# Kernel optimization log

Hardware: AMD Instinct MI355X
Metric: run time of the kernel (lower is better)

## Reference

```python
import jax, jax.numpy as jnp
import numpy as np

N_NODES = 50000
N_EDGES = 200000
IN_DIM = 16
NODE_DIM = 64
EDGE_DIM = 16
HIDDEN = 256
NUM_LAYERS = 4  # 1 NNConv + 3 GINConv


def setup_inputs() -> dict:
    key = jax.random.key(0)
    ks = jax.random.split(key, 20)
    s = 0.05
    inp = {
        "x": jax.random.normal(ks[0], (N_NODES, IN_DIM), dtype=jnp.float32),
        "edge_index": jax.random.randint(ks[1], (2, N_EDGES), 0, N_NODES, dtype=jnp.int64),
        "edge_attr": jax.random.normal(ks[2], (N_EDGES, EDGE_DIM), dtype=jnp.float32),
        # edge-NN (per-edge weight generator): attr_dim -> 256 -> 1024 -> in*out, ELU after each
        "enn_w1": jax.random.normal(ks[3], (EDGE_DIM, 256), dtype=jnp.float32) * s,
        "enn_b1": jnp.zeros((256,), dtype=jnp.float32),
        "enn_w2": jax.random.normal(ks[4], (256, 1024), dtype=jnp.float32) * s,
        "enn_b2": jnp.zeros((1024,), dtype=jnp.float32),
        "enn_w3": jax.random.normal(ks[5], (1024, IN_DIM * NODE_DIM), dtype=jnp.float32) * s,
        "enn_b3": jnp.zeros((IN_DIM * NODE_DIM,), dtype=jnp.float32),
        # NNConv root weight + bias
        "root_w": jax.random.normal(ks[6], (IN_DIM, NODE_DIM), dtype=jnp.float32) * s,
        "root_b": jnp.zeros((NODE_DIM,), dtype=jnp.float32),
        # 3 GIN MLPs (stacked): node_dim -> hidden -> hidden -> node_dim
        "gin_w1": jax.random.normal(ks[7], (3, NODE_DIM, HIDDEN), dtype=jnp.float32) * s,
        "gin_b1": jnp.zeros((3, HIDDEN), dtype=jnp.float32),
        "gin_w2": jax.random.normal(ks[8], (3, HIDDEN, HIDDEN), dtype=jnp.float32) * s,
        "gin_b2": jnp.zeros((3, HIDDEN), dtype=jnp.float32),
        "gin_w3": jax.random.normal(ks[9], (3, HIDDEN, NODE_DIM), dtype=jnp.float32) * s,
        "gin_b3": jnp.zeros((3, NODE_DIM), dtype=jnp.float32),
    }
    return inp


def _elu(x):
    return jax.nn.elu(x)


def reference(x, edge_index, edge_attr,
              enn_w1, enn_b1, enn_w2, enn_b2, enn_w3, enn_b3,
              root_w, root_b,
              gin_w1, gin_b1, gin_w2, gin_b2, gin_w3, gin_b3):
    src = edge_index[0]  # x_j (message source)
    dst = edge_index[1]  # i (aggregation target)

    # ---- Layer 0: NNConv with per-edge MLP-generated weights ----
    h = _elu(edge_attr @ enn_w1 + enn_b1)
    h = _elu(h @ enn_w2 + enn_b2)
    w_e = _elu(h @ enn_w3 + enn_b3).reshape(-1, IN_DIM, NODE_DIM)  # [E, in, out]
    msg = jnp.einsum('ei,eio->eo', x[src], w_e)                    # [E, node_dim]
    agg = jax.ops.segment_sum(msg, dst, num_segments=N_NODES)     # scatter-add
    x_cur = x @ root_w + agg + root_b                              # [N, node_dim]
    node_emb = [x_cur]

    # ---- Layers 1..3: GINConv (eps=0) with 3-layer MLP ----
    for l in range(NUM_LAYERS - 1):
        x_in = _elu(x_cur)
        nbr = jax.ops.segment_sum(x_in[src], dst, num_segments=N_NODES)
        h = x_in + nbr  # (1 + eps) * x + sum_j x_j, eps = 0
        h = _elu(h @ gin_w1[l] + gin_b1[l])
        h = _elu(h @ gin_w2[l] + gin_b2[l])
        x_cur = h @ gin_w3[l] + gin_b3[l]
        node_emb.append(x_cur)

    return jnp.stack(node_emb, axis=2)  # [N, node_dim, num_layers]
```

## Files before the change

### kernel.cpp

```cpp
#include <hip/hip_runtime.h>
#include <hip/hip_bf16.h>


#define NN 50000
#define EE 200000

typedef unsigned short u16;
typedef __attribute__((ext_vector_type(8))) short frag8;
typedef __attribute__((ext_vector_type(4))) float f32x4;

__device__ __forceinline__ float bf2f(u16 u) {
    union { unsigned int i; float f; } v; v.i = ((unsigned int)u) << 16; return v.f;
}
__device__ __forceinline__ u16 f2bf(float f) {
    union { float f; unsigned int i; } v; v.f = f;
    return (u16)((v.i + 0x7fffu + ((v.i >> 16) & 1u)) >> 16);
}
__device__ __forceinline__ float eluf(float v) {
    return v > 0.f ? v : __expf(v) - 1.f;
}

__global__ void probe_f32(const u16* __restrict__ raw, int* __restrict__ cnt) {
    int t = threadIdx.x;
    int c = 0;
    for (int j = t; j < 1024; j += 256) {
        unsigned e = (raw[j] >> 7) & 0xFF;
        if (e >= 0xBF) c++;
    }
    if (c) atomicAdd(cnt, c);
}
__global__ void cvt_bf16(const void* __restrict__ src, u16* __restrict__ dst, long n,
                         const int* __restrict__ cnt) {
    long i = (long)blockIdx.x * 256 + threadIdx.x;
    if (i >= n) return;
    if (*cnt >= 8) dst[i] = f2bf(((const float*)src)[i]);
    else           dst[i] = ((const u16*)src)[i];
}

__global__ void detect_idx64(const unsigned long long* __restrict__ p, int* __restrict__ flag) {
    long t = (long)blockIdx.x * 256 + threadIdx.x;
    if (t < EE) {
        unsigned long long v = p[t];
        if (v >> 31) atomicOr(flag, 1);
    }
}
__global__ void convert_idx(const void* __restrict__ raw, const int* __restrict__ flag,
                            int* __restrict__ s_out, int* __restrict__ d_out) {
    long t = (long)blockIdx.x * 256 + threadIdx.x;
    if (t >= EE) return;
    if (*flag) {
        const int* q = (const int*)raw;
        s_out[t] = q[t];
        d_out[t] = q[EE + t];
    } else {
        const long long* q = (const long long*)raw;
        s_out[t] = (int)q[t];
        d_out[t] = (int)q[EE + t];
    }
}

__global__ void transpose_bf16(const u16* __restrict__ in, u16* __restrict__ out, int K, int N) {
    long idx = (long)blockIdx.x * 256 + threadIdx.x;
    if (idx < (long)K * N) {
        int k = (int)(idx / N);
        int n = (int)(idx % N);
        out[(long)n * K + k] = in[idx];
    }
}

__global__ void edge_mlp1(const u16* __restrict__ attr, const u16* __restrict__ w1,
                          const u16* __restrict__ b1, u16* __restrict__ h1, int ce) {
    __shared__ u16 sa[256];
    const int t = threadIdx.x;
    const int e0 = blockIdx.x * 16;
    const int cnt = min(16, ce - e0);
    sa[t] = (t < cnt * 16) ? attr[(long)e0 * 16 + t] : (u16)0;
    float w[16];
    #pragma unroll
    for (int i = 0; i < 16; ++i) w[i] = bf2f(w1[i * 256 + t]);
    const float bb = bf2f(b1[t]);
    __syncthreads();
    for (int e = 0; e < cnt; ++e) {
        float v = bb;
        #pragma unroll
        for (int i = 0; i < 16; ++i) v += bf2f(sa[e * 16 + i]) * w[i];
        h1[(long)(e0 + e) * 256 + t] = f2bf(eluf(v));
    }
}

__device__ __forceinline__ void stage_tile(const u16* g, long row_base, long max_row,
                                           int kstride, int k0, u16* s, int t) {
    int wave = t >> 6;
    #pragma unroll
    for (int j = 0; j < 2; ++j) {
        int c = t + 256 * j;
        long r = row_base + (c >> 2);
        if (r > max_row) r = max_row;
        const u16* gp = g + r * (long)kstride + k0 + (c & 3) * 8;
        __builtin_amdgcn_global_load_lds(
            (__attribute__((address_space(1))) void*)(void*)gp,
            (__attribute__((address_space(3))) void*)((char*)s + wave * 1024 + j * 4096),
            16, 0, 0);
    }
}

__global__ __launch_bounds__(256)
void gemm_bt_bias_elu(const u16* __restrict__ A, const u16* __restrict__ BT,
                      const u16* __restrict__ bias, u16* __restrict__ C,
                      int M, int K, int N, int mpx, int lognt) {
    const int bid = blockIdx.x;
    const int xcd = bid & 7;
    const int j = bid >> 3;
    const int m_idx = xcd * mpx + (j >> lognt);
    const int n_idx = j & ((1 << lognt) - 1);
    const int num_m = (M + 127) >> 7;
    if (m_idx >= num_m) return;

    __shared__ __align__(16) u16 sA[128 * 32];
    __shared__ __align__(16) u16 sB[128 * 32];
    const int t = threadIdx.x;
    const int lane = t & 63;
    const int wave = t >> 6;
    const int wr = wave >> 1, wc = wave & 1;
    const int quad = lane >> 4, l16 = lane & 15;
    const long m0 = (long)m_idx * 128;
    const int n0 = n_idx * 128;

    f32x4 acc[4][4];
    const f32x4 z4 = {0.f, 0.f, 0.f, 0.f};
    #pragma unroll
    for (int mi = 0; mi < 4; ++mi)
        #pragma unroll
        for (int ni = 0; ni < 4; ++ni)
            acc[mi][ni] = z4;

    for (int k0 = 0; k0 < K; k0 += 32) {
        stage_tile(A, m0, (long)M - 1, K, k0, sA, t);
        stage_tile(BT, n0, (long)N - 1, K, k0, sB, t);
        __syncthreads();
        frag8 af[4], bfv[4];
        #pragma unroll
        for (int mi = 0; mi < 4; ++mi)
            af[mi] = *(const frag8*)(sA + (wr * 64 + mi * 16 + l16) * 32 + quad * 8);
        #pragma unroll
        for (int ni = 0; ni < 4; ++ni)
            bfv[ni] = *(const frag8*)(sB + (wc * 64 + ni * 16 + l16) * 32 + quad * 8);
        #pragma unroll
        for (int mi = 0; mi < 4; ++mi)
            #pragma unroll
            for (int ni = 0; ni < 4; ++ni)
                acc[mi][ni] = __builtin_amdgcn_mfma_f32_16x16x32_bf16(af[mi], bfv[ni], acc[mi][ni], 0, 0, 0);
        __syncthreads();
    }

    #pragma unroll
    for (int mi = 0; mi < 4; ++mi) {
        #pragma unroll
        for (int r = 0; r < 4; ++r) {
            long row = m0 + wr * 64 + mi * 16 + quad * 4 + r;
            if (row < M) {
                #pragma unroll
                for (int ni = 0; ni < 4; ++ni) {
                    int col = n0 + wc * 64 + ni * 16 + l16;
                    float v = acc[mi][ni][r] + bf2f(bias[col]);
                    C[row * (long)N + col] = f2bf(eluf(v));
                }
            }
        }
    }
}

__global__ __launch_bounds__(256)
void gemm_bt_f32(const u16* __restrict__ A, const u16* __restrict__ BT,
                 const u16* __restrict__ bias, float* __restrict__ C,
                 int M, int K) {
    __shared__ __align__(16) u16 sA[256 * 32];
    __shared__ __align__(16) u16 sB[64 * 32];
    const int t = threadIdx.x;
    const int lane = t & 63;
    const int wave = t >> 6;
    const int quad = lane >> 4, l16 = lane & 15;
    const long m0 = (long)blockIdx.x * 256;

    f32x4 acc[4][4];
    const f32x4 z4 = {0.f, 0.f, 0.f, 0.f};
    #pragma unroll
    for (int mi = 0; mi < 4; ++mi)
        #pragma unroll
        for (int ni = 0; ni < 4; ++ni)
            acc[mi][ni] = z4;

    for (int k0 = 0; k0 < K; k0 += 32) {
        #pragma unroll
        for (int j = 0; j < 4; ++j) {
            int c = t + 256 * j;
            long r = m0 + (c >> 2);
            if (r > (long)M - 1) r = (long)M - 1;
            const u16* gp = A + r * (long)K + k0 + (c & 3) * 8;
            __builtin_amdgcn_global_load_lds(
                (__attribute__((address_space(1))) void*)(void*)gp,
                (__attribute__((address_space(3))) void*)((char*)sA + wave * 1024 + j * 4096),
                16, 0, 0);
        }
        {
            int c = t;
            const u16* gp = BT + (long)(c >> 2) * K + k0 + (c & 3) * 8;
            __builtin_amdgcn_global_load_lds(
                (__attribute__((address_space(1))) void*)(void*)gp,
                (__attribute__((address_space(3))) void*)((char*)sB + wave * 1024),
                16, 0, 0);
        }
        __syncthreads();
        frag8 af[4], bfv[4];
        #pragma unroll
        for (int mi = 0; mi < 4; ++mi)
            af[mi] = *(const frag8*)(sA + (wave * 64 + mi * 16 + l16) * 32 + quad * 8);
        #pragma unroll
        for (int ni = 0; ni < 4; ++ni)
            bfv[ni] = *(const frag8*)(sB + (ni * 16 + l16) * 32 + quad * 8);
        #pragma unroll
        for (int mi = 0; mi < 4; ++mi)
            #pragma unroll
            for (int ni = 0; ni < 4; ++ni)
                acc[mi][ni] = __builtin_amdgcn_mfma_f32_16x16x32_bf16(af[mi], bfv[ni], acc[mi][ni], 0, 0, 0);
        __syncthreads();
    }

    #pragma unroll
    for (int mi = 0; mi < 4; ++mi) {
        #pragma unroll
        for (int r = 0; r < 4; ++r) {
            long row = m0 + wave * 64 + mi * 16 + quad * 4 + r;
            if (row < M) {
                #pragma unroll
                for (int ni = 0; ni < 4; ++ni) {
                    int col = ni * 16 + l16;
                    C[row * 64 + col] = acc[mi][ni][r] + bf2f(bias[col]);
                }
            }
        }
    }
}

__global__ void nnconv_msg(const u16* __restrict__ we, const u16* __restrict__ x,
                           const int* __restrict__ src, const int* __restrict__ dst,
                           float* __restrict__ agg, int ce) {
    long idx = (long)blockIdx.x * 256 + threadIdx.x;
    if (idx >= (long)ce * 64) return;
    int o = (int)(idx & 63);
    long e = idx >> 6;
    const u16* wr = we + e * 1024;
    const u16* xr = x + (long)src[e] * 16;
    float v = 0.f;
    #pragma unroll
    for (int i = 0; i < 16; ++i)
        v += bf2f(xr[i]) * bf2f(wr[i * 64 + o]);
    atomicAdd(&agg[(long)dst[e] * 64 + o], v);
}

__global__ void add_root(const u16* __restrict__ x, const u16* __restrict__ rw,
                         const u16* __restrict__ rb, float* __restrict__ xcur) {
    long idx = (long)blockIdx.x * 256 + threadIdx.x;
    if (idx >= (long)NN * 64) return;
    int d = (int)(idx & 63);
    long n = idx >> 6;
    float v = bf2f(rb[d]);
    #pragma unroll
    for (int i = 0; i < 16; ++i)
        v += bf2f(x[n * 16 + i]) * bf2f(rw[i * 64 + d]);
    xcur[idx] += v;
}

__global__ void elu_bf16(const float* __restrict__ in, u16* __restrict__ o, long n) {
    long idx = (long)blockIdx.x * 256 + threadIdx.x;
    if (idx < n) o[idx] = f2bf(eluf(in[idx]));
}

__global__ void gin_scatter(const u16* __restrict__ xin, const int* __restrict__ src,
                            const int* __restrict__ dst, float* __restrict__ nbr) {
    long idx = (long)blockIdx.x * 256 + threadIdx.x;
    if (idx >= (long)EE * 64) return;
    int d = (int)(idx & 63);
    long e = idx >> 6;
    atomicAdd(&nbr[(long)dst[e] * 64 + d], bf2f(xin[(long)src[e] * 64 + d]));
}

__global__ void gin_combine(const u16* __restrict__ xin, const float* __restrict__ nbr,
                            u16* __restrict__ hin, long n) {
    long idx = (long)blockIdx.x * 256 + threadIdx.x;
    if (idx < n) hin[idx] = f2bf(bf2f(xin[idx]) + nbr[idx]);
}

__global__ void write_out(const float* __restrict__ e0, const float* __restrict__ e1,
                          const float* __restrict__ e2, const float* __restrict__ e3,
                          float* __restrict__ out) {
    long idx = (long)blockIdx.x * 256 + threadIdx.x;
    if (idx >= (long)NN * 64) return;
    float4 v = {e0[idx], e1[idx], e2[idx], e3[idx]};
    *(float4*)(out + idx * 4) = v;
}

extern "C" void kernel_launch(void* const* d_in, const int* in_sizes, int n_in,
                              void* d_out, int out_size, void* d_ws, size_t ws_size,
                              hipStream_t stream) {
    (void)in_sizes; (void)n_in; (void)out_size;
    const void* eidx = d_in[1];
    float* out = (float*)d_out;

    char* ws = (char*)d_ws;
    size_t off = 0;
    auto alloc = [&](size_t bytes) {
        char* p = ws + off;
        off += (bytes + 255) & ~(size_t)255;
        return p;
    };
    int* src32 = (int*)alloc((size_t)EE * 4);
    int* dst32 = (int*)alloc((size_t)EE * 4);
    int* flag  = (int*)alloc(256);
    int* cnt   = (int*)alloc(256);
    const int cv_idx[16] = {0, 2, 3, 4, 5, 6, 7, 8, 9, 10, 11, 12, 13, 14, 15, 16};
    const long cv_n[16]  = {800000, 3200000, 4096, 256, 262144, 1024, 1048576, 1024,
                            1024, 64, 49152, 768, 196608, 768, 49152, 192};
    u16* cv[16];
    for (int i = 0; i < 16; ++i) cv[i] = (u16*)alloc((size_t)cv_n[i] * 2);
    u16 *xc = cv[0], *eac = cv[1], *w1c = cv[2], *b1c = cv[3], *w2c = cv[4], *b2c = cv[5],
        *w3c = cv[6], *b3c = cv[7], *rwc = cv[8], *rbc = cv[9],
        *g1c = cv[10], *gb1c = cv[11], *g2c = cv[12], *gb2c = cv[13], *g3c = cv[14], *gb3c = cv[15];
    u16* w2t = (u16*)alloc((size_t)1024 * 256 * 2);
    u16* w3t = (u16*)alloc((size_t)1024 * 1024 * 2);
    u16* g1t = (u16*)alloc((size_t)3 * 256 * 64 * 2);
    u16* g2t = (u16*)alloc((size_t)3 * 256 * 256 * 2);
    u16* g3t = (u16*)alloc((size_t)3 * 64 * 256 * 2);
    float* emb[4];
    for (int l = 0; l < 4; ++l) emb[l] = (float*)alloc((size_t)NN * 64 * 4);
    float* agg = emb[0];
    char* scratch = (char*)alloc(0);
    size_t avail = (ws_size > off + 4096) ? (ws_size - off - 4096) : 0;

    long CE = (long)(avail / 4608) & ~127L;
    if (CE < 128) CE = 128;
    if (CE > 200064) CE = 200064;
    u16* h1c = (u16*)scratch;
    u16* h2c = (u16*)(scratch + (size_t)CE * 512);
    u16* wec = (u16*)(scratch + (size_t)CE * 2560);

    long gin_fixed = (long)NN * 64 * 4 + (long)NN * 64 * 2;
    long gin_avail = (long)avail - gin_fixed;
    if (gin_avail < 0) gin_avail = 0;
    long CN = (gin_avail / 1152) & ~255L;
    if (CN < 256) CN = 256;
    if (CN > 50176) CN = 50176;
    float* nbr = (float*)scratch;
    u16* xin   = (u16*)(scratch + (size_t)NN * 64 * 4);
    u16* hin   = (u16*)(scratch + gin_fixed);
    u16* hg1   = hin + (size_t)CN * 64;
    u16* hg2   = hg1 + (size_t)CN * 256;

    auto cdiv = [](long a, long b) { return (unsigned)((a + b - 1) / b); };

    hipMemsetAsync(cnt, 0, 4, stream);
    probe_f32<<<1, 256, 0, stream>>>((const u16*)d_in[0], cnt);
    for (int i = 0; i < 16; ++i)
        cvt_bf16<<<cdiv(cv_n[i], 256), 256, 0, stream>>>(d_in[cv_idx[i]], cv[i], cv_n[i], cnt);

    hipMemsetAsync(flag, 0, 4, stream);
    detect_idx64<<<cdiv(EE, 256), 256, 0, stream>>>((const unsigned long long*)eidx, flag);
    convert_idx<<<cdiv(EE, 256), 256, 0, stream>>>(eidx, flag, src32, dst32);

    transpose_bf16<<<cdiv(256 * 1024, 256), 256, 0, stream>>>(w2c, w2t, 256, 1024);
    transpose_bf16<<<cdiv(1024 * 1024, 256), 256, 0, stream>>>(w3c, w3t, 1024, 1024);
    for (int l = 0; l < 3; ++l) {
        transpose_bf16<<<cdiv(64 * 256, 256), 256, 0, stream>>>(g1c + l * 64 * 256, g1t + l * 256 * 64, 64, 256);
        transpose_bf16<<<cdiv(256 * 256, 256), 256, 0, stream>>>(g2c + l * 256 * 256, g2t + l * 256 * 256, 256, 256);
        transpose_bf16<<<cdiv(256 * 64, 256), 256, 0, stream>>>(g3c + l * 256 * 64, g3t + l * 64 * 256, 256, 64);
    }

    hipMemsetAsync(agg, 0, (size_t)NN * 64 * 4, stream);
    for (long e0 = 0; e0 < EE; e0 += CE) {
        int ce = (int)((EE - e0 < CE) ? (EE - e0) : CE);
        int mpx = cdiv(cdiv(ce, 128), 8);
        edge_mlp1<<<cdiv(ce, 16), 256, 0, stream>>>(eac + e0 * 16, w1c, b1c, h1c, ce);
        gemm_bt_bias_elu<<<8 * mpx * 8, 256, 0, stream>>>(h1c, w2t, b2c, h2c, ce, 256, 1024, mpx, 3);
        gemm_bt_bias_elu<<<8 * mpx * 8, 256, 0, stream>>>(h2c, w3t, b3c, wec, ce, 1024, 1024, mpx, 3);
        nnconv_msg<<<cdiv((long)ce * 64, 256), 256, 0, stream>>>(wec, xc, src32 + e0, dst32 + e0, agg, ce);
    }
    add_root<<<cdiv((long)NN * 64, 256), 256, 0, stream>>>(xc, rwc, rbc, agg);

    for (int l = 0; l < 3; ++l) {
        elu_bf16<<<cdiv((long)NN * 64, 256), 256, 0, stream>>>(emb[l], xin, (long)NN * 64);
        hipMemsetAsync(nbr, 0, (size_t)NN * 64 * 4, stream);
        gin_scatter<<<cdiv((long)EE * 64, 256), 256, 0, stream>>>(xin, src32, dst32, nbr);
        for (long n0 = 0; n0 < NN; n0 += CN) {
            int cn = (int)((NN - n0 < CN) ? (NN - n0) : CN);
            int mpx = cdiv(cdiv(cn, 128), 8);
            gin_combine<<<cdiv((long)cn * 64, 256), 256, 0, stream>>>(xin + n0 * 64, nbr + n0 * 64, hin, (long)cn * 64);
            gemm_bt_bias_elu<<<8 * mpx * 2, 256, 0, stream>>>(hin, g1t + l * 256 * 64, gb1c + l * 256, hg1, cn, 64, 256, mpx, 1);
            gemm_bt_bias_elu<<<8 * mpx * 2, 256, 0, stream>>>(hg1, g2t + l * 256 * 256, gb2c + l * 256, hg2, cn, 256, 256, mpx, 1);
            gemm_bt_f32<<<cdiv(cn, 256), 256, 0, stream>>>(hg2, g3t + l * 64 * 256, gb3c + l * 64, emb[l + 1] + n0 * 64, cn, 256);
        }
    }
    write_out<<<cdiv((long)NN * 64, 256), 256, 0, stream>>>(emb[0], emb[1], emb[2], emb[3], out);
}
```

Before: 1.611 ms.

## Use 256x256-tile triple-buffered GEMM with direct-to-LDS loads for edge MLP

Adds a new GEMM kernel with 256x256 output tiles, 512 threads and a three-stage LDS ring filled by global_load_lds. It also uses swizzled LDS addressing and raises wave priority around the MFMA block. It replaces the 128-tile GEMMs for the two large per-edge MLP layers, aiming for more operand reuse per load and better overlap of memory with compute. The cost is heavier register and LDS use per block (about 96KB LDS), which lowers occupancy, and fewer blocks per chunk, which risks under-filling the GPU.

```diff
diff --git a/kernel.cpp b/kernel.cpp
--- a/kernel.cpp
+++ b/kernel.cpp
@@ -162,6 +162,118 @@
                 #pragma unroll
                 for (int ni = 0; ni < 4; ++ni) {
                     int col = n0 + wc * 64 + ni * 16 + l16;
+                    float v = acc[mi][ni][r] + bf2f(bias[col]);
+                    C[row * (long)N + col] = f2bf(eluf(v));
+                }
+            }
+        }
+    }
+}
+
+__global__ __launch_bounds__(512)
+void gemm256(const u16* __restrict__ A, const u16* __restrict__ BT,
+             const u16* __restrict__ bias, u16* __restrict__ C,
+             int M, int K, int N, int mpx, int lognt) {
+    const int bid = blockIdx.x;
+    const int xcd = bid & 7;
+    const int j = bid >> 3;
+    const int m_idx = xcd * mpx + (j >> lognt);
+    const int n_idx = j & ((1 << lognt) - 1);
+    const int num_m = (M + 255) >> 8;
+    if (m_idx >= num_m) return;
+
+    __shared__ __align__(16) u16 sA[3][256 * 32];
+    __shared__ __align__(16) u16 sB[3][256 * 32];
+    const int t = threadIdx.x;
+    const int lane = t & 63;
+    const int wave = t >> 6;
+    const int wm = wave >> 2;
+    const int wn = wave & 3;
+    const int quad = lane >> 4, l16 = lane & 15;
+    const long m0 = (long)m_idx * 256;
+    const int n0 = n_idx * 256;
+
+    const int rowin = lane >> 2;
+    const int slotp = (((lane & 3) ^ ((lane >> 3) & 3)) << 3);
+
+    const int rsw = (quad ^ ((l16 >> 1) & 3)) << 4;
+    const int aoff = (wm * 128 + l16) * 64 + rsw;
+    const int boff = (wn * 64 + l16) * 64 + rsw;
+
+    const int ntk = K >> 5;
+
+    auto stage = [&](int kt, int bf_) {
+        #pragma unroll
+        for (int jj = 0; jj < 2; ++jj) {
+            const int ck = wave * 2 + jj;
+            long r = m0 + ck * 16 + rowin;
+            if (r > (long)M - 1) r = (long)M - 1;
+            const u16* gp = A + r * (long)K + (kt << 5) + slotp;
+            __builtin_amdgcn_global_load_lds(
+                (__attribute__((address_space(1))) void*)(void*)gp,
+                (__attribute__((address_space(3))) void*)((char*)sA[bf_] + ck * 1024),
+                16, 0, 0);
+        }
+        #pragma unroll
+        for (int jj = 0; jj < 2; ++jj) {
+            const int ck = wave * 2 + jj;
+            long r = n0 + ck * 16 + rowin;
+            if (r > (long)N - 1) r = (long)N - 1;
+            const u16* gp = BT + r * (long)K + (kt << 5) + slotp;
+            __builtin_amdgcn_global_load_lds(
+                (__attribute__((address_space(1))) void*)(void*)gp,
+                (__attribute__((address_space(3))) void*)((char*)sB[bf_] + ck * 1024),
+                16, 0, 0);
+        }
+    };
+
+    f32x4 acc[8][4];
+    const f32x4 z4 = {0.f, 0.f, 0.f, 0.f};
+    #pragma unroll
+    for (int mi = 0; mi < 8; ++mi)
+        #pragma unroll
+        for (int ni = 0; ni < 4; ++ni)
+            acc[mi][ni] = z4;
+
+    stage(0, 0);
+    if (ntk > 1) stage(1, 1);
+
+    int buf = 0;
+    for (int kt = 0; kt < ntk; ++kt) {
+        if (kt + 1 < ntk) asm volatile("s_waitcnt vmcnt(4)" ::: "memory");
+        else              asm volatile("s_waitcnt vmcnt(0)" ::: "memory");
+        __builtin_amdgcn_s_barrier();
+        __builtin_amdgcn_sched_barrier(0);
+        if (kt + 2 < ntk) stage(kt + 2, buf == 0 ? 2 : buf - 1);
+
+        const u16* pa = sA[buf];
+        const u16* pb = sB[buf];
+        frag8 af[8], bfv[4];
+        #pragma unroll
+        for (int mi = 0; mi < 8; ++mi)
+            af[mi] = *(const frag8*)((const char*)pa + aoff + mi * 1024);
+        #pragma unroll
+        for (int ni = 0; ni < 4; ++ni)
+            bfv[ni] = *(const frag8*)((const char*)pb + boff + ni * 1024);
+        __builtin_amdgcn_s_setprio(1);
+        #pragma unroll
+        for (int mi = 0; mi < 8; ++mi)
+            #pragma unroll
+            for (int ni = 0; ni < 4; ++ni)
+                acc[mi][ni] = __builtin_amdgcn_mfma_f32_16x16x32_bf16(af[mi], bfv[ni], acc[mi][ni], 0, 0, 0);
+        __builtin_amdgcn_s_setprio(0);
+        buf = (buf == 2) ? 0 : buf + 1;
+    }
+
+    #pragma unroll
+    for (int mi = 0; mi < 8; ++mi) {
+        #pragma unroll
+        for (int r = 0; r < 4; ++r) {
+            long row = m0 + wm * 128 + mi * 16 + quad * 4 + r;
+            if (row < M) {
+                #pragma unroll
+                for (int ni = 0; ni < 4; ++ni) {
+                    int col = n0 + wn * 64 + ni * 16 + l16;
                     float v = acc[mi][ni][r] + bf2f(bias[col]);
                     C[row * (long)N + col] = f2bf(eluf(v));
                 }
@@ -378,10 +490,10 @@
     hipMemsetAsync(agg, 0, (size_t)NN * 64 * 4, stream);
     for (long e0 = 0; e0 < EE; e0 += CE) {
         int ce = (int)((EE - e0 < CE) ? (EE - e0) : CE);
-        int mpx = cdiv(cdiv(ce, 128), 8);
+        int mpx2 = cdiv(cdiv(ce, 256), 8);
         edge_mlp1<<<cdiv(ce, 16), 256, 0, stream>>>(eac + e0 * 16, w1c, b1c, h1c, ce);
-        gemm_bt_bias_elu<<<8 * mpx * 8, 256, 0, stream>>>(h1c, w2t, b2c, h2c, ce, 256, 1024, mpx, 3);
-        gemm_bt_bias_elu<<<8 * mpx * 8, 256, 0, stream>>>(h2c, w3t, b3c, wec, ce, 1024, 1024, mpx, 3);
+        gemm256<<<8 * mpx2 * 4, 512, 0, stream>>>(h1c, w2t, b2c, h2c, ce, 256, 1024, mpx2, 2);
+        gemm256<<<8 * mpx2 * 4, 512, 0, stream>>>(h2c, w3t, b3c, wec, ce, 1024, 1024, mpx2, 2);
         nnconv_msg<<<cdiv((long)ce * 64, 256), 256, 0, stream>>>(wec, xc, src32 + e0, dst32 + e0, agg, ce);
     }
     add_root<<<cdiv((long)NN * 64, 256), 256, 0, stream>>>(xc, rwc, rbc, agg);
```

Result: slower. 1.682 ms (+4.4%).

## Add 256x256-tile pipelined MFMA GEMM for edge-MLP layers

Applied to the files above, without the earlier changes.

Adds a new 512-thread GEMM kernel with 256x256 output tiles. It loads directly from global memory into LDS with an XOR swizzle, double-buffers the K tiles, and interleaves loads with MFMA phases using barriers and s_setprio. The kernel replaces the 128-tile GEMM for the two large per-edge weight-generator matmuls (256->1024 and 1024->1024). The aim is more data reuse per block and better overlap of global loads with MFMA work on the dominant compute stage. In exchange it relies on delicate manual vmcnt/barrier scheduling, which could cause hazards or register spills.

```diff
diff --git a/kernel.cpp b/kernel.cpp
--- a/kernel.cpp
+++ b/kernel.cpp
@@ -162,6 +162,155 @@
                 #pragma unroll
                 for (int ni = 0; ni < 4; ++ni) {
                     int col = n0 + wc * 64 + ni * 16 + l16;
+                    float v = acc[mi][ni][r] + bf2f(bias[col]);
+                    C[row * (long)N + col] = f2bf(eluf(v));
+                }
+            }
+        }
+    }
+}
+
+
+#define QPHASE(PA, PB, QM, QN, LDA, LDB, STREG, SG, SRBASE, SRMAX, SKT, VMW)     \
+  do {                                                                           \
+    if (LDA) {                                                                   \
+      _Pragma("unroll")                                                          \
+      for (int mi = 0; mi < 4; ++mi) {                                           \
+        _Pragma("unroll")                                                        \
+        for (int kk = 0; kk < 2; ++kk) {                                         \
+          int row = ((QM) * 4 + mi) * 16 + l16;                                  \
+          int slot = ((kk << 2) + quad) ^ (l16 & 7);                             \
+          av[mi][kk] = *(const frag8*)((const char*)(PA) + row * 128 + slot * 16); \
+        }                                                                        \
+      }                                                                          \
+    }                                                                            \
+    if ((LDB) >= 0) {                                                            \
+      _Pragma("unroll")                                                          \
+      for (int ni = 0; ni < 2; ++ni) {                                           \
+        _Pragma("unroll")                                                        \
+        for (int kk = 0; kk < 2; ++kk) {                                         \
+          int row = (wn & 1) * 64 + (((LDB) & 1) * 2 + ni) * 16 + l16;           \
+          int slot = ((kk << 2) + quad) ^ (l16 & 7);                             \
+          bv[(LDB) & 1][ni][kk] =                                                \
+              *(const frag8*)((const char*)(PB) + row * 128 + slot * 16);        \
+        }                                                                        \
+      }                                                                          \
+    }                                                                            \
+    stage((STREG), (SG), (SRBASE), (SRMAX), (SKT));                              \
+    if (VMW) asm volatile("s_waitcnt vmcnt(4)" ::: "memory");                    \
+    __builtin_amdgcn_s_barrier();                                                \
+    asm volatile("s_waitcnt lgkmcnt(0)" ::: "memory");                           \
+    __builtin_amdgcn_sched_barrier(0);                                           \
+    __builtin_amdgcn_s_setprio(1);                                               \
+    _Pragma("unroll")                                                            \
+    for (int kk = 0; kk < 2; ++kk) {                                             \
+      _Pragma("unroll")                                                          \
+      for (int mi = 0; mi < 4; ++mi) {                                           \
+        _Pragma("unroll")                                                        \
+        for (int ni = 0; ni < 2; ++ni) {                                         \
+          acc[(QM) * 4 + mi][(QN) * 2 + ni] =                                    \
+              __builtin_amdgcn_mfma_f32_16x16x32_bf16(                           \
+                  av[mi][kk], bv[(QN)][ni][kk],                                  \
+                  acc[(QM) * 4 + mi][(QN) * 2 + ni], 0, 0, 0);                   \
+        }                                                                        \
+      }                                                                          \
+    }                                                                            \
+    __builtin_amdgcn_s_setprio(0);                                               \
+    __builtin_amdgcn_s_barrier();                                                \
+    __builtin_amdgcn_sched_barrier(0);                                           \
+  } while (0)
+
+__global__ __launch_bounds__(512, 2)
+void gemm256p(const u16* __restrict__ A, const u16* __restrict__ BT,
+              const u16* __restrict__ bias, u16* __restrict__ C,
+              int M, int K, int N, int mpx, int lognt) {
+    const int bid = blockIdx.x;
+    const int xcd = bid & 7;
+    const int j = bid >> 3;
+    const int m_idx = xcd * mpx + (j >> lognt);
+    const int n_idx = j & ((1 << lognt) - 1);
+    const int num_m = (M + 255) >> 8;
+    if (m_idx >= num_m) return;
+
+    __shared__ __align__(16) u16 lds[2][4][8192];
+    const int t = threadIdx.x;
+    const int lane = t & 63;
+    const int wave = t >> 6;
+    const int wm = wave >> 2;
+    const int wn = wave & 3;
+    const int quad = lane >> 4, l16 = lane & 15;
+    const long m0 = (long)m_idx * 256;
+    const long n0 = (long)n_idx * 256;
+
+    const int gslot = (((lane & 7) ^ ((lane >> 3) & 7)) << 3);
+
+    auto stage = [&](u16* reg, const u16* G, long rbase, long rmax, int kt) {
+        #pragma unroll
+        for (int jj = 0; jj < 2; ++jj) {
+            const int ck = wave * 2 + jj;
+            long r = rbase + ck * 8 + (lane >> 3);
+            if (r > rmax) r = rmax;
+            const u16* gp = G + r * (long)K + ((long)kt << 6) + gslot;
+            __builtin_amdgcn_global_load_lds(
+                (__attribute__((address_space(1))) void*)(void*)gp,
+                (__attribute__((address_space(3))) void*)((char*)reg + ck * 1024),
+                16, 0, 0);
+        }
+    };
+
+    f32x4 acc[8][4];
+    const f32x4 z4 = {0.f, 0.f, 0.f, 0.f};
+    #pragma unroll
+    for (int mi = 0; mi < 8; ++mi)
+        #pragma unroll
+        for (int ni = 0; ni < 4; ++ni)
+            acc[mi][ni] = z4;
+    frag8 av[4][2];
+    frag8 bv[2][2][2];
+
+    const int ntk = K >> 6;
+    const int niter = ntk >> 1;
+    const long MM = (long)M - 1, NMX = (long)N - 1;
+
+    stage(&lds[0][2][0], BT, n0,       NMX, 0);
+    stage(&lds[0][3][0], BT, n0 + 128, NMX, 0);
+    stage(&lds[0][0][0], A,  m0,       MM,  0);
+    stage(&lds[0][1][0], A,  m0 + 128, MM,  0);
+    stage(&lds[1][2][0], BT, n0,       NMX, 1);
+    stage(&lds[1][3][0], BT, n0 + 128, NMX, 1);
+    asm volatile("s_waitcnt vmcnt(4)" ::: "memory");
+    __builtin_amdgcn_s_barrier();
+
+    const u16* paX = &lds[0][wm][0];
+    const u16* pbX = &lds[0][2 + (wn >> 1)][0];
+    const u16* paY = &lds[1][wm][0];
+    const u16* pbY = &lds[1][2 + (wn >> 1)][0];
+
+    for (int it = 0; it < niter; ++it) {
+        const int t1k = 2 * it + 1;
+        int t2k = 2 * it + 2; if (t2k > ntk - 1) t2k = ntk - 1;
+        int t3k = 2 * it + 3; if (t3k > ntk - 1) t3k = ntk - 1;
+
+        QPHASE(paX, pbX, 0, 0, 1,  0, &lds[1][0][0], A,  m0,       MM,  t1k, 0);
+        QPHASE(paX, pbX, 0, 1, 0,  1, &lds[1][1][0], A,  m0 + 128, MM,  t1k, 0);
+        QPHASE(paX, pbX, 1, 0, 1, -1, &lds[0][2][0], BT, n0,       NMX, t2k, 0);
+        QPHASE(paX, pbX, 1, 1, 0, -1, &lds[0][3][0], BT, n0 + 128, NMX, t2k, 1);
+        QPHASE(paY, pbY, 0, 0, 1,  0, &lds[0][0][0], A,  m0,       MM,  t2k, 0);
+        QPHASE(paY, pbY, 0, 1, 0,  1, &lds[0][1][0], A,  m0 + 128, MM,  t2k, 0);
+        QPHASE(paY, pbY, 1, 0, 1, -1, &lds[1][2][0], BT, n0,       NMX, t3k, 0);
+        QPHASE(paY, pbY, 1, 1, 0, -1, &lds[1][3][0], BT, n0 + 128, NMX, t3k, 1);
+    }
+    asm volatile("s_waitcnt vmcnt(0)" ::: "memory");
+
+    #pragma unroll
+    for (int mi = 0; mi < 8; ++mi) {
+        #pragma unroll
+        for (int r = 0; r < 4; ++r) {
+            long row = m0 + wm * 128 + mi * 16 + quad * 4 + r;
+            if (row < M) {
+                #pragma unroll
+                for (int ni = 0; ni < 4; ++ni) {
+                    long col = n0 + wn * 64 + ni * 16 + l16;
                     float v = acc[mi][ni][r] + bf2f(bias[col]);
                     C[row * (long)N + col] = f2bf(eluf(v));
                 }
@@ -378,10 +527,10 @@
     hipMemsetAsync(agg, 0, (size_t)NN * 64 * 4, stream);
     for (long e0 = 0; e0 < EE; e0 += CE) {
         int ce = (int)((EE - e0 < CE) ? (EE - e0) : CE);
-        int mpx = cdiv(cdiv(ce, 128), 8);
+        int mpx2 = cdiv(cdiv(ce, 256), 8);
         edge_mlp1<<<cdiv(ce, 16), 256, 0, stream>>>(eac + e0 * 16, w1c, b1c, h1c, ce);
-        gemm_bt_bias_elu<<<8 * mpx * 8, 256, 0, stream>>>(h1c, w2t, b2c, h2c, ce, 256, 1024, mpx, 3);
-        gemm_bt_bias_elu<<<8 * mpx * 8, 256, 0, stream>>>(h2c, w3t, b3c, wec, ce, 1024, 1024, mpx, 3);
+        gemm256p<<<8 * mpx2 * 4, 512, 0, stream>>>(h1c, w2t, b2c, h2c, ce, 256, 1024, mpx2, 2);
+        gemm256p<<<8 * mpx2 * 4, 512, 0, stream>>>(h2c, w3t, b3c, wec, ce, 1024, 1024, mpx2, 2);
         nnconv_msg<<<cdiv((long)ce * 64, 256), 256, 0, stream>>>(wec, xc, src32 + e0, dst32 + e0, agg, ce);
     }
     add_root<<<cdiv((long)NN * 64, 256), 256, 0, stream>>>(xc, rwc, rbc, agg);
```

After: 1.553 ms. 3.6% less time.
